# Kernel optimization log

Hardware: AMD Instinct MI355X
Metric: run time of the kernel (lower is better)

The kernel has to match this reference:

```python
import jax, jax.numpy as jnp
import numpy as np

EMBED_DIM = 1024
NUM_HEADS = 16
D_K = EMBED_DIM // NUM_HEADS


def setup_inputs() -> dict:
    key = jax.random.key(0)
    kx, kq, kk, kv, ko = jax.random.split(key, 5)
    scale = 1.0 / np.sqrt(EMBED_DIM)
    x = jax.random.normal(kx, (4, 2048, EMBED_DIM), dtype=jnp.float32)
    # Linear(embed_dim, embed_dim, bias=False) weights, stored [out, in] like torch
    Wq = jax.random.uniform(kq, (EMBED_DIM, EMBED_DIM), jnp.float32, -scale, scale)
    Wk = jax.random.uniform(kk, (EMBED_DIM, EMBED_DIM), jnp.float32, -scale, scale)
    Wv = jax.random.uniform(kv, (EMBED_DIM, EMBED_DIM), jnp.float32, -scale, scale)
    Wo = jax.random.uniform(ko, (EMBED_DIM, EMBED_DIM), jnp.float32, -scale, scale)
    return {"x": x, "Wq": Wq, "Wk": Wk, "Wv": Wv, "Wo": Wo}


def reference(x, Wq, Wk, Wv, Wo):
    b, s, _ = x.shape
    # torch Linear: y = x @ W.T
    def proj(W):
        y = jnp.einsum('bse,fe->bsf', x, W)
        return y.reshape(b, s, NUM_HEADS, D_K).transpose(0, 2, 1, 3)  # [b,h,s,d]
    q, k, v = proj(Wq), proj(Wk), proj(Wv)
    scores = jnp.einsum('bhqd,bhkd->bhqk', q, k) / jnp.sqrt(jnp.float32(D_K))
    attn = jax.nn.softmax(scores, axis=-1)  # dropout is identity in eval
    out = jnp.einsum('bhqk,bhkd->bhqd', attn, v)
    out = out.transpose(0, 2, 1, 3).reshape(b, s, EMBED_DIM)
    return jnp.einsum('bsf,ef->bse', out, Wo)
```

## Files before the change

kernel.cpp:

```cpp
#include <hip/hip_runtime.h>
#include <hip/hip_bf16.h>

typedef unsigned short u16;
typedef unsigned int   u32;
typedef __attribute__((ext_vector_type(8))) __bf16 bf16x8;
typedef __attribute__((ext_vector_type(2))) __bf16 bf16x2;
typedef __attribute__((ext_vector_type(8))) u16    ushort8v;
typedef __attribute__((ext_vector_type(2))) float  f32x2;
typedef __attribute__((ext_vector_type(4))) float  floatx4;

#define EMBED 1024
#define SEQ   2048
#define BATCH 4
#define NH    16
#define DKH   64
#define BHN   (BATCH*NH)
#define ZSTRIDE ((size_t)BHN*SEQ*DKH)

__device__ __forceinline__ u16 f2bf(float f){
  union { float f; unsigned u; } v; v.f = f;
  unsigned r = (v.u + 0x7FFFu + ((v.u >> 16) & 1u)) >> 16;
  return (u16)r;
}
__device__ __forceinline__ u32 pk2(float a, float b){
  f32x2 v = {a, b};
  return __builtin_bit_cast(u32, __builtin_convertvector(v, bf16x2));
}

__device__ __forceinline__ bf16x8 ld_frag(const u16* p){
  return __builtin_bit_cast(bf16x8, *(const ushort8v*)p);
}

__device__ __forceinline__ floatx4 mfma16(bf16x8 a, bf16x8 b, floatx4 c){
  return __builtin_amdgcn_mfma_f32_16x16x32_bf16(a, b, c, 0, 0, 0);
}

__device__ __forceinline__ void gl_lds16(const u16* g, u16* l){
  __builtin_amdgcn_global_load_lds((const __attribute__((address_space(1))) void*)g,
                                   (__attribute__((address_space(3))) void*)l,
                                   16, 0, 0);
}

__global__ __launch_bounds__(256) void cvt_all(const float* __restrict__ x,
    const float* __restrict__ wq, const float* __restrict__ wk,
    const float* __restrict__ wv, const float* __restrict__ wo,
    u16* __restrict__ Xb, u16* __restrict__ Wqb, u16* __restrict__ Wkb,
    u16* __restrict__ Wvb, u16* __restrict__ Wob){
  int b = blockIdx.x;
  const float* src; u16* dst; int i;
  if (b < 8192){ src = x; dst = Xb; i = b*256 + threadIdx.x; }
  else {
    int k = (b - 8192) >> 10, r = (b - 8192) & 1023;
    src = (k==0) ? wq : (k==1) ? wk : (k==2) ? wv : wo;
    dst = (k==0) ? Wqb : (k==1) ? Wkb : (k==2) ? Wvb : Wob;
    i = r*256 + threadIdx.x;
  }
  float4 v = ((const float4*)src)[i];
  ushort4 o;
  o.x = f2bf(v.x); o.y = f2bf(v.y); o.z = f2bf(v.z); o.w = f2bf(v.w);
  ((ushort4*)dst)[i] = o;
}

#define QSCALE 0.1803368801111204f
__global__ __launch_bounds__(256, 2) void gemm_qkv(const u16* __restrict__ X,
    const u16* __restrict__ Wq, const u16* __restrict__ Wk, const u16* __restrict__ Wv,
    u16* __restrict__ QKV){
  __shared__ __attribute__((aligned(16))) u16 As[2*128*32];
  __shared__ __attribute__((aligned(16))) u16 Bs[3][2*128*32];

  const int tid = threadIdx.x, lane = tid & 63, w = tid >> 6;
  const int lm = lane & 15, quad = lane >> 4;
  const int wm = (w & 1) * 64, wn = (w >> 1) * 64;
  const int m0 = blockIdx.x * 128, n0 = blockIdx.y * 128;
  const int row0 = tid >> 2, kc = tid & 3;

  const u16* A0 = X  + (size_t)(m0 + row0)*EMBED + kc*8;
  const u16* B0[3] = {
    Wq + (size_t)(n0 + row0)*EMBED + kc*8,
    Wk + (size_t)(n0 + row0)*EMBED + kc*8,
    Wv + (size_t)(n0 + row0)*EMBED + kc*8 };

  floatx4 acc[3][4][4];
  #pragma unroll
  for (int z = 0; z < 3; ++z)
    #pragma unroll
    for (int mi = 0; mi < 4; ++mi)
      #pragma unroll
      for (int ni = 0; ni < 4; ++ni)
        acc[z][mi][ni] = (floatx4){0.f, 0.f, 0.f, 0.f};

  gl_lds16(A0,            As + tid*8);
  gl_lds16(A0 + 64*EMBED, As + (256 + tid)*8);
  #pragma unroll
  for (int z = 0; z < 3; ++z){
    gl_lds16(B0[z],            Bs[z] + tid*8);
    gl_lds16(B0[z] + 64*EMBED, Bs[z] + (256 + tid)*8);
  }

  for (int kt = 0; kt < EMBED/32; ++kt){
    const int cur = kt & 1;
    __syncthreads();
    if (kt + 1 < EMBED/32){
      const int k0 = (kt + 1) * 32;
      gl_lds16(A0 + k0,            As + (cur^1)*4096 + tid*8);
      gl_lds16(A0 + 64*EMBED + k0, As + (cur^1)*4096 + (256 + tid)*8);
      #pragma unroll
      for (int z = 0; z < 3; ++z){
        gl_lds16(B0[z] + k0,            Bs[z] + (cur^1)*4096 + tid*8);
        gl_lds16(B0[z] + 64*EMBED + k0, Bs[z] + (cur^1)*4096 + (256 + tid)*8);
      }
    }
    const u16* Ac = As + cur*4096;
    bf16x8 af[4];
    #pragma unroll
    for (int mi = 0; mi < 4; ++mi)
      af[mi] = ld_frag(&Ac[(wm + mi*16 + lm)*32 + quad*8]);
    #pragma unroll
    for (int z = 0; z < 3; ++z){
      const u16* Bc = Bs[z] + cur*4096;
      bf16x8 bfz[4];
      #pragma unroll
      for (int ni = 0; ni < 4; ++ni)
        bfz[ni] = ld_frag(&Bc[(wn + ni*16 + lm)*32 + quad*8]);
      #pragma unroll
      for (int mi = 0; mi < 4; ++mi)
        #pragma unroll
        for (int ni = 0; ni < 4; ++ni)
          acc[z][mi][ni] = mfma16(af[mi], bfz[ni], acc[z][mi][ni]);
    }
  }

  #pragma unroll
  for (int z = 0; z < 2; ++z){
    const float scale = (z == 0) ? QSCALE : 1.0f;
    u16* outz = QKV + (size_t)z * ZSTRIDE;
    #pragma unroll
    for (int mi = 0; mi < 4; ++mi)
      #pragma unroll
      for (int ni = 0; ni < 4; ++ni)
        #pragma unroll
        for (int r = 0; r < 4; ++r){
          int m = m0 + wm + mi*16 + quad*4 + r;
          int n = n0 + wn + ni*16 + lm;
          int b = m >> 11, s = m & 2047, h = n >> 6, d = n & 63;
          outz[(((size_t)(b*NH + h))*SEQ + s)*DKH + d] = f2bf(acc[z][mi][ni][r] * scale);
        }
  }
  {
    u16* outz = QKV + (size_t)2 * ZSTRIDE;
    #pragma unroll
    for (int mi = 0; mi < 4; ++mi)
      #pragma unroll
      for (int ni = 0; ni < 4; ++ni){
        int mbase = m0 + wm + mi*16 + quad*4;
        int n = n0 + wn + ni*16 + lm;
        int b = mbase >> 11, sb = mbase & 2047;
        int h = n >> 6, d = n & 63;
        u16* dst = outz + (((size_t)(b*NH + h))*DKH + d)*SEQ + sb;
        uint2 pv;
        pv.x = pk2(acc[2][mi][ni][0], acc[2][mi][ni][1]);
        pv.y = pk2(acc[2][mi][ni][2], acc[2][mi][ni][3]);
        *reinterpret_cast<uint2*>(dst) = pv;
      }
  }
}

__global__ __launch_bounds__(256) void gemm_out(const u16* __restrict__ A,
    const u16* __restrict__ W, float* __restrict__ C){
  __shared__ __attribute__((aligned(16))) u16 As[2*128*64];
  __shared__ __attribute__((aligned(16))) u16 Bs[2*128*64];
  const int tid = threadIdx.x, lane = tid & 63, w = tid >> 6;
  const int lm = lane & 15, quad = lane >> 4;
  const int wm = (w & 1) * 64, wn = (w >> 1) * 64;
  const int m0 = blockIdx.x * 128, n0 = blockIdx.y * 128;

  const int srow = tid >> 3;
  const int ssw  = ((tid & 7) ^ (srow & 7)) * 8;
  const u16* Ab = A + (size_t)(m0 + srow)*EMBED + ssw;
  const u16* Bb = W + (size_t)(n0 + srow)*EMBED + ssw;

  floatx4 acc[4][4];
  #pragma unroll
  for (int mi = 0; mi < 4; ++mi)
    #pragma unroll
    for (int ni = 0; ni < 4; ++ni)
      acc[mi][ni] = (floatx4){0.f, 0.f, 0.f, 0.f};

  #pragma unroll
  for (int j = 0; j < 4; ++j){
    gl_lds16(Ab + (size_t)j*32*EMBED, As + (j*256 + tid)*8);
    gl_lds16(Bb + (size_t)j*32*EMBED, Bs + (j*256 + tid)*8);
  }

  for (int kt = 0; kt < EMBED/64; ++kt){
    const int cur = kt & 1;
    __syncthreads();
    if (kt + 1 < EMBED/64){
      const int k0 = (kt + 1) * 64;
      #pragma unroll
      for (int j = 0; j < 4; ++j){
        gl_lds16(Ab + (size_t)j*32*EMBED + k0, As + (cur^1)*8192 + (j*256 + tid)*8);
        gl_lds16(Bb + (size_t)j*32*EMBED + k0, Bs + (cur^1)*8192 + (j*256 + tid)*8);
      }
    }
    const u16* Ac = As + cur*8192;
    const u16* Bc = Bs + cur*8192;
    #pragma unroll
    for (int kh = 0; kh < 2; ++kh){
      const int us = ((kh*4 + quad) ^ (lm & 7)) * 8;
      bf16x8 af[4], bf[4];
      #pragma unroll
      for (int mi = 0; mi < 4; ++mi)
        af[mi] = ld_frag(&Ac[(wm + mi*16 + lm)*64 + us]);
      #pragma unroll
      for (int ni = 0; ni < 4; ++ni)
        bf[ni] = ld_frag(&Bc[(wn + ni*16 + lm)*64 + us]);
      #pragma unroll
      for (int mi = 0; mi < 4; ++mi)
        #pragma unroll
        for (int ni = 0; ni < 4; ++ni)
          acc[mi][ni] = mfma16(af[mi], bf[ni], acc[mi][ni]);
    }
  }

  #pragma unroll
  for (int mi = 0; mi < 4; ++mi)
    #pragma unroll
    for (int ni = 0; ni < 4; ++ni)
      #pragma unroll
      for (int r = 0; r < 4; ++r){
        int m = m0 + wm + mi*16 + quad*4 + r;
        int n = n0 + wn + ni*16 + lm;
        C[(size_t)m*EMBED + n] = acc[mi][ni][r];
      }
}

#define KSS 520
__global__ __launch_bounds__(256, 4) void attn_kernel(const u16* __restrict__ QKV,
                                                      u16* __restrict__ Out){
  __shared__ __attribute__((aligned(16))) u16 Ks[2][8*KSS];
  __shared__ __attribute__((aligned(16))) u16 Vs[2][64*64];

  const int tid = threadIdx.x, lane = tid & 63, w = tid >> 6;
  const int lm = lane & 15, quad = lane >> 4;
  const int bh = blockIdx.x;
  const int q0 = blockIdx.y * 128;
  const u16* Qh = QKV + (size_t)bh * SEQ * DKH;
  const u16* Kh = QKV + ZSTRIDE + (size_t)bh * SEQ * DKH;
  const u16* Vh = QKV + 2*ZSTRIDE + (size_t)bh * DKH * SEQ;

  const int sK = tid & 63, cK = tid >> 6;
  const int dV = tid >> 3, gV = tid & 7;
  const size_t vsrc0 = (size_t)dV * SEQ + ((gV ^ (dV & 7)) * 8);
  const size_t vsrc1 = vsrc0 + (size_t)32 * SEQ;

  bf16x8 qf[2][2];
  #pragma unroll
  for (int qt = 0; qt < 2; ++qt)
    #pragma unroll
    for (int st = 0; st < 2; ++st)
      qf[qt][st] = ld_frag(Qh + (size_t)(q0 + w*32 + qt*16 + lm)*DKH + st*32 + quad*8);

  const uint4 ONESW = {0x3F803F80u, 0x3F803F80u, 0x3F803F80u, 0x3F803F80u};
  const bf16x8 ones8 = __builtin_bit_cast(bf16x8, ONESW);

  floatx4 o[2][4], lac[2];
  #pragma unroll
  for (int qt = 0; qt < 2; ++qt){
    lac[qt] = (floatx4){0.f, 0.f, 0.f, 0.f};
    #pragma unroll
    for (int dt = 0; dt < 4; ++dt) o[qt][dt] = (floatx4){0.f, 0.f, 0.f, 0.f};
  }

  gl_lds16(Kh + (size_t)sK*DKH + cK*8,     Ks[0] + cK*KSS + sK*8);
  gl_lds16(Kh + (size_t)sK*DKH + (cK+4)*8, Ks[0] + (cK+4)*KSS + sK*8);
  gl_lds16(Vh + vsrc0,                     Vs[0] + tid*8);
  gl_lds16(Vh + vsrc1,                     Vs[0] + 2048 + tid*8);

  for (int kt = 0; kt < SEQ/64; ++kt){
    const int cur = kt & 1;
    __syncthreads();
    if (kt + 1 < SEQ/64){
      const int nk0 = (kt + 1) * 64;
      gl_lds16(Kh + (size_t)(nk0 + sK)*DKH + cK*8,     Ks[cur^1] + cK*KSS + sK*8);
      gl_lds16(Kh + (size_t)(nk0 + sK)*DKH + (cK+4)*8, Ks[cur^1] + (cK+4)*KSS + sK*8);
      gl_lds16(Vh + vsrc0 + nk0,                       Vs[cur^1] + tid*8);
      gl_lds16(Vh + vsrc1 + nk0,                       Vs[cur^1] + 2048 + tid*8);
    }
    const u16* Kc = Ks[cur];
    const u16* Vc = Vs[cur];

    #pragma unroll
    for (int u = 0; u < 2; ++u){
      uint2 ph[2][2];
      #pragma unroll
      for (int half = 0; half < 2; ++half){
        const int t = u*2 + half;
        bf16x8 kf0 = ld_frag(&Kc[quad*KSS     + (t*16 + lm)*8]);
        bf16x8 kf1 = ld_frag(&Kc[(quad+4)*KSS + (t*16 + lm)*8]);
        #pragma unroll
        for (int qt = 0; qt < 2; ++qt){
          floatx4 s = (floatx4){0.f,0.f,0.f,0.f};
          __builtin_amdgcn_s_setprio(1);
          s = mfma16(kf0, qf[qt][0], s);
          s = mfma16(kf1, qf[qt][1], s);
          __builtin_amdgcn_s_setprio(0);
          ph[qt][half].x = pk2(__builtin_amdgcn_exp2f(s[0]), __builtin_amdgcn_exp2f(s[1]));
          ph[qt][half].y = pk2(__builtin_amdgcn_exp2f(s[2]), __builtin_amdgcn_exp2f(s[3]));
        }
      }
      bf16x8 pf[2];
      #pragma unroll
      for (int qt = 0; qt < 2; ++qt){
        uint4 pp = {ph[qt][0].x, ph[qt][0].y, ph[qt][1].x, ph[qt][1].y};
        pf[qt] = __builtin_bit_cast(bf16x8, pp);
      }
      const int cg0 = (((u*4     + (quad >> 1)) ^ (lm & 7)) * 8) + (quad & 1) * 4;
      const int cg1 = (((u*4 + 2 + (quad >> 1)) ^ (lm & 7)) * 8) + (quad & 1) * 4;
      __builtin_amdgcn_s_setprio(1);
      lac[0] = mfma16(pf[0], ones8, lac[0]);
      lac[1] = mfma16(pf[1], ones8, lac[1]);
      #pragma unroll
      for (int dt = 0; dt < 4; ++dt){
        uint2 vlo = *(const uint2*)(Vc + (dt*16 + lm)*64 + cg0);
        uint2 vhi = *(const uint2*)(Vc + (dt*16 + lm)*64 + cg1);
        uint4 vv = {vlo.x, vlo.y, vhi.x, vhi.y};
        bf16x8 vb = __builtin_bit_cast(bf16x8, vv);
        o[0][dt] = mfma16(pf[0], vb, o[0][dt]);
        o[1][dt] = mfma16(pf[1], vb, o[1][dt]);
      }
      __builtin_amdgcn_s_setprio(0);
    }
  }

  const int bI = bh >> 4, h = bh & 15;
  #pragma unroll
  for (int qt = 0; qt < 2; ++qt){
    floatx4 inv;
    #pragma unroll
    for (int r = 0; r < 4; ++r) inv[r] = __builtin_amdgcn_rcpf(lac[qt][r]);
    #pragma unroll
    for (int dt = 0; dt < 4; ++dt)
      #pragma unroll
      for (int r = 0; r < 4; ++r){
        int s = q0 + w*32 + qt*16 + quad*4 + r;
        Out[((size_t)(bI*SEQ + s))*EMBED + h*DKH + dt*16 + lm] = f2bf(o[qt][dt][r] * inv[r]);
      }
  }
}

extern "C" void kernel_launch(void* const* d_in, const int* in_sizes, int n_in,
                              void* d_out, int out_size, void* d_ws, size_t ws_size,
                              hipStream_t stream){
  const float* x  = (const float*)d_in[0];
  const float* Wq = (const float*)d_in[1];
  const float* Wk = (const float*)d_in[2];
  const float* Wv = (const float*)d_in[3];
  const float* Wo = (const float*)d_in[4];
  float* out = (float*)d_out;

  char* ws = (char*)d_ws;
  u16* Xb  = (u16*)ws;
  u16* Wqb = (u16*)(ws + (size_t)16777216);
  u16* Wkb = Wqb + 1048576;
  u16* Wvb = Wkb + 1048576;
  u16* Wob = Wvb + 1048576;
  u16* QKV = (u16*)(ws + (size_t)25165824);
  u16* At  = (u16*)(ws + (size_t)75497472);

  cvt_all<<<12288, 256, 0, stream>>>(x, Wq, Wk, Wv, Wo, Xb, Wqb, Wkb, Wvb, Wob);
  gemm_qkv<<<dim3(64, 8), 256, 0, stream>>>(Xb, Wqb, Wkb, Wvb, QKV);
  attn_kernel<<<dim3(64, 16), 256, 0, stream>>>(QKV, At);
  gemm_out<<<dim3(64, 8), 256, 0, stream>>>(At, Wob, out);
}
```

Measured before the change: 250.8 us.

## Split barriers with explicit vmcnt waits and double attention query tile per block

Replaces __syncthreads with raw s_barrier plus explicit s_waitcnt vmcnt, so only the older double-buffer loads are waited on and the just-issued prefetch stays in flight across the compute step. The attention kernel now handles 256 queries per block (64 per wave), which halves the grid and reuses each loaded K/V tile across twice as many queries. It also drops the s_setprio hints and lowers launch bounds to 2 blocks per CU. More accumulator registers per wave may cut occupancy, and fewer blocks may leave CUs underused. The hand-counted vmcnt values must match the number of outstanding loads or correctness breaks.

```diff
diff --git a/kernel.cpp b/kernel.cpp
--- a/kernel.cpp
+++ b/kernel.cpp
@@ -40,6 +40,8 @@
                                    (__attribute__((address_space(3))) void*)l,
                                    16, 0, 0);
 }
+
+#define CFENCE asm volatile("" ::: "memory")
 
 __global__ __launch_bounds__(256) void cvt_all(const float* __restrict__ x,
     const float* __restrict__ wq, const float* __restrict__ wk,
@@ -99,7 +101,8 @@
 
   for (int kt = 0; kt < EMBED/32; ++kt){
     const int cur = kt & 1;
-    __syncthreads();
+    __builtin_amdgcn_s_barrier();
+    CFENCE;
     if (kt + 1 < EMBED/32){
       const int k0 = (kt + 1) * 32;
       gl_lds16(A0 + k0,            As + (cur^1)*4096 + tid*8);
@@ -109,7 +112,12 @@
         gl_lds16(B0[z] + k0,            Bs[z] + (cur^1)*4096 + tid*8);
         gl_lds16(B0[z] + 64*EMBED + k0, Bs[z] + (cur^1)*4096 + (256 + tid)*8);
       }
-    }
+      asm volatile("s_waitcnt vmcnt(8)" ::: "memory");
+    } else {
+      asm volatile("s_waitcnt vmcnt(0)" ::: "memory");
+    }
+    __builtin_amdgcn_s_barrier();
+    CFENCE;
     const u16* Ac = As + cur*4096;
     bf16x8 af[4];
     #pragma unroll
@@ -194,7 +202,8 @@
 
   for (int kt = 0; kt < EMBED/64; ++kt){
     const int cur = kt & 1;
-    __syncthreads();
+    __builtin_amdgcn_s_barrier();
+    CFENCE;
     if (kt + 1 < EMBED/64){
       const int k0 = (kt + 1) * 64;
       #pragma unroll
@@ -202,7 +211,12 @@
         gl_lds16(Ab + (size_t)j*32*EMBED + k0, As + (cur^1)*8192 + (j*256 + tid)*8);
         gl_lds16(Bb + (size_t)j*32*EMBED + k0, Bs + (cur^1)*8192 + (j*256 + tid)*8);
       }
-    }
+      asm volatile("s_waitcnt vmcnt(8)" ::: "memory");
+    } else {
+      asm volatile("s_waitcnt vmcnt(0)" ::: "memory");
+    }
+    __builtin_amdgcn_s_barrier();
+    CFENCE;
     const u16* Ac = As + cur*8192;
     const u16* Bc = Bs + cur*8192;
     #pragma unroll
@@ -236,7 +250,7 @@
 }
 
 #define KSS 520
-__global__ __launch_bounds__(256, 4) void attn_kernel(const u16* __restrict__ QKV,
+__global__ __launch_bounds__(256, 2) void attn_kernel(const u16* __restrict__ QKV,
                                                       u16* __restrict__ Out){
   __shared__ __attribute__((aligned(16))) u16 Ks[2][8*KSS];
   __shared__ __attribute__((aligned(16))) u16 Vs[2][64*64];
@@ -244,7 +258,7 @@
   const int tid = threadIdx.x, lane = tid & 63, w = tid >> 6;
   const int lm = lane & 15, quad = lane >> 4;
   const int bh = blockIdx.x;
-  const int q0 = blockIdx.y * 128;
+  const int q0 = blockIdx.y * 256;
   const u16* Qh = QKV + (size_t)bh * SEQ * DKH;
   const u16* Kh = QKV + ZSTRIDE + (size_t)bh * SEQ * DKH;
   const u16* Vh = QKV + 2*ZSTRIDE + (size_t)bh * DKH * SEQ;
@@ -254,19 +268,19 @@
   const size_t vsrc0 = (size_t)dV * SEQ + ((gV ^ (dV & 7)) * 8);
   const size_t vsrc1 = vsrc0 + (size_t)32 * SEQ;
 
-  bf16x8 qf[2][2];
-  #pragma unroll
-  for (int qt = 0; qt < 2; ++qt)
+  bf16x8 qf[4][2];
+  #pragma unroll
+  for (int qt = 0; qt < 4; ++qt)
     #pragma unroll
     for (int st = 0; st < 2; ++st)
-      qf[qt][st] = ld_frag(Qh + (size_t)(q0 + w*32 + qt*16 + lm)*DKH + st*32 + quad*8);
+      qf[qt][st] = ld_frag(Qh + (size_t)(q0 + w*64 + qt*16 + lm)*DKH + st*32 + quad*8);
 
   const uint4 ONESW = {0x3F803F80u, 0x3F803F80u, 0x3F803F80u, 0x3F803F80u};
   const bf16x8 ones8 = __builtin_bit_cast(bf16x8, ONESW);
 
-  floatx4 o[2][4], lac[2];
-  #pragma unroll
-  for (int qt = 0; qt < 2; ++qt){
+  floatx4 o[4][4], lac[4];
+  #pragma unroll
+  for (int qt = 0; qt < 4; ++qt){
     lac[qt] = (floatx4){0.f, 0.f, 0.f, 0.f};
     #pragma unroll
     for (int dt = 0; dt < 4; ++dt) o[qt][dt] = (floatx4){0.f, 0.f, 0.f, 0.f};
@@ -279,63 +293,67 @@
 
   for (int kt = 0; kt < SEQ/64; ++kt){
     const int cur = kt & 1;
-    __syncthreads();
+    __builtin_amdgcn_s_barrier();
+    CFENCE;
     if (kt + 1 < SEQ/64){
       const int nk0 = (kt + 1) * 64;
       gl_lds16(Kh + (size_t)(nk0 + sK)*DKH + cK*8,     Ks[cur^1] + cK*KSS + sK*8);
       gl_lds16(Kh + (size_t)(nk0 + sK)*DKH + (cK+4)*8, Ks[cur^1] + (cK+4)*KSS + sK*8);
       gl_lds16(Vh + vsrc0 + nk0,                       Vs[cur^1] + tid*8);
       gl_lds16(Vh + vsrc1 + nk0,                       Vs[cur^1] + 2048 + tid*8);
-    }
+      asm volatile("s_waitcnt vmcnt(4)" ::: "memory");
+    } else {
+      asm volatile("s_waitcnt vmcnt(0)" ::: "memory");
+    }
+    __builtin_amdgcn_s_barrier();
+    CFENCE;
     const u16* Kc = Ks[cur];
     const u16* Vc = Vs[cur];
 
     #pragma unroll
     for (int u = 0; u < 2; ++u){
-      uint2 ph[2][2];
+      uint2 e[4][2];
       #pragma unroll
       for (int half = 0; half < 2; ++half){
         const int t = u*2 + half;
         bf16x8 kf0 = ld_frag(&Kc[quad*KSS     + (t*16 + lm)*8]);
         bf16x8 kf1 = ld_frag(&Kc[(quad+4)*KSS + (t*16 + lm)*8]);
         #pragma unroll
-        for (int qt = 0; qt < 2; ++qt){
+        for (int qt = 0; qt < 4; ++qt){
           floatx4 s = (floatx4){0.f,0.f,0.f,0.f};
-          __builtin_amdgcn_s_setprio(1);
           s = mfma16(kf0, qf[qt][0], s);
           s = mfma16(kf1, qf[qt][1], s);
-          __builtin_amdgcn_s_setprio(0);
-          ph[qt][half].x = pk2(__builtin_amdgcn_exp2f(s[0]), __builtin_amdgcn_exp2f(s[1]));
-          ph[qt][half].y = pk2(__builtin_amdgcn_exp2f(s[2]), __builtin_amdgcn_exp2f(s[3]));
+          e[qt][half].x = pk2(__builtin_amdgcn_exp2f(s[0]), __builtin_amdgcn_exp2f(s[1]));
+          e[qt][half].y = pk2(__builtin_amdgcn_exp2f(s[2]), __builtin_amdgcn_exp2f(s[3]));
         }
       }
-      bf16x8 pf[2];
-      #pragma unroll
-      for (int qt = 0; qt < 2; ++qt){
-        uint4 pp = {ph[qt][0].x, ph[qt][0].y, ph[qt][1].x, ph[qt][1].y};
+      bf16x8 pf[4];
+      #pragma unroll
+      for (int qt = 0; qt < 4; ++qt){
+        uint4 pp = {e[qt][0].x, e[qt][0].y, e[qt][1].x, e[qt][1].y};
         pf[qt] = __builtin_bit_cast(bf16x8, pp);
       }
+      #pragma unroll
+      for (int qt = 0; qt < 4; ++qt)
+        lac[qt] = mfma16(pf[qt], ones8, lac[qt]);
       const int cg0 = (((u*4     + (quad >> 1)) ^ (lm & 7)) * 8) + (quad & 1) * 4;
       const int cg1 = (((u*4 + 2 + (quad >> 1)) ^ (lm & 7)) * 8) + (quad & 1) * 4;
-      __builtin_amdgcn_s_setprio(1);
-      lac[0] = mfma16(pf[0], ones8, lac[0]);
-      lac[1] = mfma16(pf[1], ones8, lac[1]);
       #pragma unroll
       for (int dt = 0; dt < 4; ++dt){
         uint2 vlo = *(const uint2*)(Vc + (dt*16 + lm)*64 + cg0);
         uint2 vhi = *(const uint2*)(Vc + (dt*16 + lm)*64 + cg1);
         uint4 vv = {vlo.x, vlo.y, vhi.x, vhi.y};
         bf16x8 vb = __builtin_bit_cast(bf16x8, vv);
-        o[0][dt] = mfma16(pf[0], vb, o[0][dt]);
-        o[1][dt] = mfma16(pf[1], vb, o[1][dt]);
-      }
-      __builtin_amdgcn_s_setprio(0);
+        #pragma unroll
+        for (int qt = 0; qt < 4; ++qt)
+          o[qt][dt] = mfma16(pf[qt], vb, o[qt][dt]);
+      }
     }
   }
 
   const int bI = bh >> 4, h = bh & 15;
   #pragma unroll
-  for (int qt = 0; qt < 2; ++qt){
+  for (int qt = 0; qt < 4; ++qt){
     floatx4 inv;
     #pragma unroll
     for (int r = 0; r < 4; ++r) inv[r] = __builtin_amdgcn_rcpf(lac[qt][r]);
@@ -343,7 +361,7 @@
     for (int dt = 0; dt < 4; ++dt)
       #pragma unroll
       for (int r = 0; r < 4; ++r){
-        int s = q0 + w*32 + qt*16 + quad*4 + r;
+        int s = q0 + w*64 + qt*16 + quad*4 + r;
         Out[((size_t)(bI*SEQ + s))*EMBED + h*DKH + dt*16 + lm] = f2bf(o[qt][dt][r] * inv[r]);
       }
   }
@@ -370,6 +388,6 @@
 
   cvt_all<<<12288, 256, 0, stream>>>(x, Wq, Wk, Wv, Wo, Xb, Wqb, Wkb, Wvb, Wob);
   gemm_qkv<<<dim3(64, 8), 256, 0, stream>>>(Xb, Wqb, Wkb, Wvb, QKV);
-  attn_kernel<<<dim3(64, 16), 256, 0, stream>>>(QKV, At);
+  attn_kernel<<<dim3(64, 8), 256, 0, stream>>>(QKV, At);
   gemm_out<<<dim3(64, 8), 256, 0, stream>>>(At, Wob, out);
 }
```

Result: no change. 247.3 us (-1.4%).
